# Kernel optimization log

Measured on AMD Instinct MI355X. Metric: run time of the kernel, lower is better.

The kernel has to match this reference:

```python
import jax, jax.numpy as jnp
import numpy as np

SIGMA = 1.2
SIGMA_SQ = jnp.float32(SIGMA * SIGMA)


def setup_inputs() -> dict:
    key = jax.random.key(0)
    k1, k2, k3 = jax.random.split(key, 3)
    X = jax.random.normal(k1, (32768, 2), dtype=jnp.float32)
    pattern_layer = jax.random.normal(k2, (8192, 2), dtype=jnp.float32)
    W2 = jax.random.normal(k3, (8192,), dtype=jnp.float32)
    return {"X": X, "pattern_layer": pattern_layer, "W2": W2}


def reference(X, pattern_layer, W2):
    # Pairwise squared distances via |a|^2 + |b|^2 - 2 a.b  -> [N, P]
    x_sq = jnp.sum(X * X, axis=1, keepdims=True)              # [N, 1]
    p_sq = jnp.sum(pattern_layer * pattern_layer, axis=1)     # [P]
    cross = X @ pattern_layer.T                               # [N, P]
    Dsq = x_sq + p_sq[None, :] - 2.0 * cross                  # [N, P]
    K = jnp.exp(-Dsq / (2.0 * SIGMA_SQ))                      # RBF kernel [N, P]
    num = K @ W2                                              # [N]
    den = jnp.sum(K, axis=1)                                  # [N]
    return num / den
```

## Files before the change

kernel.cpp:

```cpp
#include <hip/hip_runtime.h>

#define N 32768
#define P 8192
#define MX 8
#define XG 2
#define PH 2
#define THREADS (XG * PH * 64)
#define XPB (XG * MX)
#define NBLK (N / XPB)
#define PATS_PER_PH (P / PH)
#define QITERS (PATS_PER_PH / 2)
#define ITERS (QITERS / 64)

#define RBF_F 0.50093577808645257f

static __device__ __forceinline__ float fast_exp2(float x) {
#if __has_builtin(__builtin_amdgcn_exp2f)
    return __builtin_amdgcn_exp2f(x);
#else
    return exp2f(x);
#endif
}

static __device__ __forceinline__ float exp2_poly(float t) {
    float u = t + 12582912.0f;
    int   iu = __float_as_int(u);
    float r = u - 12582912.0f;
    float f = t - r;
    float p = fmaf(f, 0.00961812910f, 0.05550410866f);
    p = fmaf(f, p, 0.24022650696f);
    p = fmaf(f, p, 0.69314718056f);
    p = fmaf(f, p, 1.0f);
    float s = __int_as_float((int)(((unsigned)iu << 23) + 0x3F800000u));
    return p * s;
}

__global__ void prep_kernel(const float* __restrict__ pat,
                            const float* __restrict__ w2,
                            float4* __restrict__ c) {
    int i = blockIdx.x * blockDim.x + threadIdx.x;
    if (i < P) {
        float p0 = pat[2 * i];
        float p1 = pat[2 * i + 1];
        float4 v;
        v.x = 2.0f * RBF_F * p0;
        v.y = 2.0f * RBF_F * p1;
        v.z = -RBF_F * (p0 * p0 + p1 * p1);
        v.w = w2[i];
        c[i] = v;
    }
}

__global__ __launch_bounds__(THREADS) void
rbf_kernel(const float* __restrict__ X,
           const float4* __restrict__ c,
           float* __restrict__ out) {
    const int t    = threadIdx.x;
    const int lane = t & 63;
    const int w    = __builtin_amdgcn_readfirstlane(t >> 6);
    const int xg   = w >> 1;
    const int ph   = w & 1;

    const int xb = blockIdx.x * XPB + xg * MX;
    const float2* Xp = (const float2*)X;
    float x0[MX], x1[MX];
#pragma unroll
    for (int i = 0; i < MX; ++i) {
        float2 xv = Xp[xb + i];
        x0[i] = xv.x;
        x1[i] = xv.y;
    }

    float num[MX], den[MX];
#pragma unroll
    for (int i = 0; i < MX; ++i) { num[i] = 0.f; den[i] = 0.f; }

    const float4* __restrict__ C4 = c + (size_t)ph * PATS_PER_PH;

    float4 a = C4[2 * lane];
    float4 b = C4[2 * lane + 1];

    for (int j = 0; j < ITERS; ++j) {
        const int qn = (((j + 1) & (ITERS - 1)) << 6) + lane;
        float4 an = C4[2 * qn];
        float4 bn = C4[2 * qn + 1];

#pragma unroll
        for (int i = 0; i < MX; ++i) {
            float ta = fmaf(a.y, x1[i], fmaf(a.x, x0[i], a.z));
            float tb = fmaf(b.y, x1[i], fmaf(b.x, x0[i], b.z));
            float ka, kb;
            if ((i & 3) == 3) {
                ka = exp2_poly(ta);
                kb = exp2_poly(tb);
            } else {
                ka = fast_exp2(ta);
                kb = fast_exp2(tb);
            }
            den[i] += ka;
            num[i] = fmaf(ka, a.w, num[i]);
            den[i] += kb;
            num[i] = fmaf(kb, b.w, num[i]);
        }
        a = an;
        b = bn;
    }

#pragma unroll
    for (int m = 1; m < 64; m <<= 1) {
#pragma unroll
        for (int i = 0; i < MX; ++i) {
            num[i] += __shfl_xor(num[i], m, 64);
            den[i] += __shfl_xor(den[i], m, 64);
        }
    }

    __shared__ float red[XG][PH][MX][2];
    if (lane == 0) {
#pragma unroll
        for (int i = 0; i < MX; ++i) {
            red[xg][ph][i][0] = num[i];
            red[xg][ph][i][1] = den[i];
        }
    }
    __syncthreads();

    if (t < XPB) {
        int g = t >> 3, xi = t & 7;
        float nn = red[g][0][xi][0] + red[g][1][xi][0];
        float dd = red[g][0][xi][1] + red[g][1][xi][1];
        out[blockIdx.x * XPB + t] = nn / dd;
    }
}

extern "C" void kernel_launch(void* const* d_in, const int* in_sizes, int n_in,
                              void* d_out, int out_size, void* d_ws, size_t ws_size,
                              hipStream_t stream) {
    const float* X   = (const float*)d_in[0];
    const float* pat = (const float*)d_in[1];
    const float* w2  = (const float*)d_in[2];
    float* out = (float*)d_out;
    float4* c = (float4*)d_ws;

    prep_kernel<<<(P + 255) / 256, 256, 0, stream>>>(pat, w2, c);
    rbf_kernel<<<NBLK, THREADS, 0, stream>>>(X, c, out);
}
```

Before: 108.1 us.

## Use fp16 dot2 for RBF exponent argument and double-buffer pattern loads

Packs the scaled pattern coordinates into fp16 pairs and converts X to fp16 so each exponent argument is computed with a single v_dot2 instruction with fp32 accumulation instead of two FMAs. It drops the mixed polynomial exp2 path and uses the hardware exp2 for all rows. It also unrolls the pattern loop by two with a two-deep prefetch of pattern data to hide load latency. The fp16 coordinates lose precision in the exponent argument, which may raise output error.

```diff
diff --git a/kernel.cpp b/kernel.cpp
--- a/kernel.cpp
+++ b/kernel.cpp
@@ -9,10 +9,11 @@
 #define XPB (XG * MX)
 #define NBLK (N / XPB)
 #define PATS_PER_PH (P / PH)
-#define QITERS (PATS_PER_PH / 2)
-#define ITERS (QITERS / 64)
+#define ITERS (PATS_PER_PH / 128)
 
 #define RBF_F 0.50093577808645257f
+
+typedef _Float16 h2 __attribute__((ext_vector_type(2)));
 
 static __device__ __forceinline__ float fast_exp2(float x) {
 #if __has_builtin(__builtin_amdgcn_exp2f)
@@ -22,17 +23,13 @@
 #endif
 }
 
-static __device__ __forceinline__ float exp2_poly(float t) {
-    float u = t + 12582912.0f;
-    int   iu = __float_as_int(u);
-    float r = u - 12582912.0f;
-    float f = t - r;
-    float p = fmaf(f, 0.00961812910f, 0.05550410866f);
-    p = fmaf(f, p, 0.24022650696f);
-    p = fmaf(f, p, 0.69314718056f);
-    p = fmaf(f, p, 1.0f);
-    float s = __int_as_float((int)(((unsigned)iu << 23) + 0x3F800000u));
-    return p * s;
+static __device__ __forceinline__ float dot2(float c01, h2 xh, float c2) {
+#if __has_builtin(__builtin_amdgcn_fdot2)
+    return __builtin_amdgcn_fdot2(__builtin_bit_cast(h2, c01), xh, c2, false);
+#else
+    h2 cc = __builtin_bit_cast(h2, c01);
+    return fmaf((float)cc.x, (float)xh.x, fmaf((float)cc.y, (float)xh.y, c2));
+#endif
 }
 
 __global__ void prep_kernel(const float* __restrict__ pat,
@@ -42,11 +39,14 @@
     if (i < P) {
         float p0 = pat[2 * i];
         float p1 = pat[2 * i + 1];
+        h2 hh;
+        hh.x = (_Float16)(2.0f * RBF_F * p0);
+        hh.y = (_Float16)(2.0f * RBF_F * p1);
         float4 v;
-        v.x = 2.0f * RBF_F * p0;
-        v.y = 2.0f * RBF_F * p1;
-        v.z = -RBF_F * (p0 * p0 + p1 * p1);
-        v.w = w2[i];
+        v.x = __builtin_bit_cast(float, hh);
+        v.y = -RBF_F * (p0 * p0 + p1 * p1);
+        v.z = w2[i];
+        v.w = 0.0f;
         c[i] = v;
     }
 }
@@ -63,12 +63,14 @@
 
     const int xb = blockIdx.x * XPB + xg * MX;
     const float2* Xp = (const float2*)X;
-    float x0[MX], x1[MX];
+    h2 xh[MX];
 #pragma unroll
     for (int i = 0; i < MX; ++i) {
         float2 xv = Xp[xb + i];
-        x0[i] = xv.x;
-        x1[i] = xv.y;
+        h2 hv;
+        hv.x = (_Float16)xv.x;
+        hv.y = (_Float16)xv.y;
+        xh[i] = hv;
     }
 
     float num[MX], den[MX];
@@ -77,33 +79,40 @@
 
     const float4* __restrict__ C4 = c + (size_t)ph * PATS_PER_PH;
 
-    float4 a = C4[2 * lane];
-    float4 b = C4[2 * lane + 1];
-
-    for (int j = 0; j < ITERS; ++j) {
-        const int qn = (((j + 1) & (ITERS - 1)) << 6) + lane;
-        float4 an = C4[2 * qn];
-        float4 bn = C4[2 * qn + 1];
-
+    auto compute = [&](const float4& A, const float4& B) {
 #pragma unroll
         for (int i = 0; i < MX; ++i) {
-            float ta = fmaf(a.y, x1[i], fmaf(a.x, x0[i], a.z));
-            float tb = fmaf(b.y, x1[i], fmaf(b.x, x0[i], b.z));
-            float ka, kb;
-            if ((i & 3) == 3) {
-                ka = exp2_poly(ta);
-                kb = exp2_poly(tb);
-            } else {
-                ka = fast_exp2(ta);
-                kb = fast_exp2(tb);
-            }
+            float ta = dot2(A.x, xh[i], A.y);
+            float tb = dot2(B.x, xh[i], B.y);
+            float ka = fast_exp2(ta);
+            float kb = fast_exp2(tb);
             den[i] += ka;
-            num[i] = fmaf(ka, a.w, num[i]);
+            num[i] = fmaf(ka, A.z, num[i]);
             den[i] += kb;
-            num[i] = fmaf(kb, b.w, num[i]);
+            num[i] = fmaf(kb, B.z, num[i]);
         }
-        a = an;
-        b = bn;
+    };
+
+    float4 a0 = C4[(0 << 7) + 2 * lane];
+    float4 b0 = C4[(0 << 7) + 2 * lane + 1];
+    float4 a1 = C4[(1 << 7) + 2 * lane];
+    float4 b1 = C4[(1 << 7) + 2 * lane + 1];
+
+    for (int j = 0; j < ITERS; j += 2) {
+        {
+            const int j2 = (j + 2) & (ITERS - 1);
+            float4 na = C4[(j2 << 7) + 2 * lane];
+            float4 nb = C4[(j2 << 7) + 2 * lane + 1];
+            compute(a0, b0);
+            a0 = na; b0 = nb;
+        }
+        {
+            const int j3 = (j + 3) & (ITERS - 1);
+            float4 na = C4[(j3 << 7) + 2 * lane];
+            float4 nb = C4[(j3 << 7) + 2 * lane + 1];
+            compute(a1, b1);
+            a1 = na; b1 = nb;
+        }
     }
 
 #pragma unroll
```

New measurement: 98.58 us. 1.1x faster.
